# Optimization experiments

Hardware: AMD Instinct MI355X
Metric: run time of the kernel (lower is better)

Reference implementation:

```python
import jax, jax.numpy as jnp
import numpy as np

EMBED_DIM = 1024
NUM_HEADS = 16
HEAD_DIM = EMBED_DIM // NUM_HEADS
# Source divides by scale = head_dim**-0.5, i.e. multiplies logits by sqrt(head_dim).
INV_SCALE = float(HEAD_DIM) ** 0.5


def setup_inputs() -> dict:
    key = jax.random.key(0)
    ks = jax.random.split(key, 9)
    E = EMBED_DIM
    s = 1.0 / np.sqrt(E)
    x = jax.random.normal(ks[0], (2, 2048, E), dtype=jnp.float32)
    Wq = jax.random.uniform(ks[1], (E, E), jnp.float32, -s, s)
    bq = jax.random.uniform(ks[2], (E,), jnp.float32, -s, s)
    Wk = jax.random.uniform(ks[3], (E, E), jnp.float32, -s, s)
    bk = jax.random.uniform(ks[4], (E,), jnp.float32, -s, s)
    Wv = jax.random.uniform(ks[5], (E, E), jnp.float32, -s, s)
    bv = jax.random.uniform(ks[6], (E,), jnp.float32, -s, s)
    Wo = jax.random.uniform(ks[7], (E, E), jnp.float32, -s, s)
    bo = jax.random.uniform(ks[8], (E,), jnp.float32, -s, s)
    return {"x": x, "Wq": Wq, "bq": bq, "Wk": Wk, "bk": bk,
            "Wv": Wv, "bv": bv, "Wo": Wo, "bo": bo}


def reference(x, Wq, bq, Wk, bk, Wv, bv, Wo, bo):
    B, N, C = x.shape
    H, D = NUM_HEADS, HEAD_DIM
    # nn.Linear: y = x @ W.T + b
    q = (x @ Wq.T + bq).reshape(B, N, H, D).transpose(0, 2, 1, 3)  # [B,H,N,D]
    k = (x @ Wk.T + bk).reshape(B, N, H, D).transpose(0, 2, 1, 3)
    v = (x @ Wv.T + bv).reshape(B, N, H, D).transpose(0, 2, 1, 3)
    # Faithful to source: logits = QK^T / (head_dim**-0.5) = QK^T * sqrt(head_dim)
    logits = jnp.einsum('bhnd,bhmd->bhnm', q, k) * INV_SCALE  # [B,H,N,N]
    attn = jax.nn.softmax(logits, axis=-1)
    h = jnp.einsum('bhnm,bhmd->bhnd', attn, v)  # [B,H,N,D]
    concat_h = h.transpose(0, 2, 1, 3).reshape(B, N, C)
    return concat_h @ Wo.T + bo
```

## Files before the change

kernel.cpp:

```cpp
#include <hip/hip_runtime.h>
#include <math.h>

#define B_ 2
#define N_ 2048
#define E_ 1024
#define H_ 16
#define D_ 64

typedef unsigned short US;
typedef _Float16 h16x8 __attribute__((ext_vector_type(8)));
typedef _Float16 h16x4 __attribute__((ext_vector_type(4)));
typedef __fp16 fp16x2 __attribute__((ext_vector_type(2)));
typedef float f32x4 __attribute__((ext_vector_type(4)));
#define MFMA16F(a,b,c)  __builtin_amdgcn_mfma_f32_16x16x32_f16(a,b,c,0,0,0)
#define MFMA161(a,b,c)  __builtin_amdgcn_mfma_f32_16x16x16f16(a,b,c,0,0,0)
#define SCL  11.5415603828f

union HU { _Float16 h; US u; };
__device__ __forceinline__ US f2h(float f){ HU x; x.h = (_Float16)f; return x.u; }
__device__ __forceinline__ unsigned pkrtz(float a, float b){
  union { fp16x2 h; unsigned u; } x;
  x.h = __builtin_amdgcn_cvt_pkrtz(a, b);
  return x.u;
}

union U8 { US u[8]; uint4 v; };
union U4 { US u[4]; uint2 v; };
union UPA { unsigned u[2]; h16x4 h; };

__device__ __forceinline__ void glds16(const US* g, US* l){
  __builtin_amdgcn_global_load_lds(
    (const __attribute__((address_space(1))) unsigned int*)(const void*)g,
    (__attribute__((address_space(3))) unsigned int*)(void*)l, 16, 0, 0);
}

__global__ __launch_bounds__(256) void conv_all(
    const float* __restrict__ x,
    const float* __restrict__ w0, const float* __restrict__ w1,
    const float* __restrict__ w2, const float* __restrict__ w3,
    US* __restrict__ xh, US* __restrict__ Wall)
{
  const int id = blockIdx.x;
  const float* s; US* d; size_t off;
  if (id < 2048) { s = x; d = xh; off = (size_t)id*2048; }
  else {
    int j = id - 2048, wsel = j>>9;
    off = (size_t)(j&511)*2048;
    s = (wsel==0)?w0:(wsel==1)?w1:(wsel==2)?w2:w3;
    d = Wall + (size_t)wsel*1048576;
  }
  size_t i = off + (size_t)threadIdx.x*8;
  float f[8];
  *(float4*)&f[0] = *(const float4*)&s[i];
  *(float4*)&f[4] = *(const float4*)&s[i+4];
  U8 h;
  #pragma unroll
  for (int j=0;j<8;++j) h.u[j] = f2h(f[j]);
  *(uint4*)&d[i] = h.v;
}

__global__ __launch_bounds__(256,3) void qkv_gemm(
    const US* __restrict__ A, const US* __restrict__ Wall,
    const float* __restrict__ bq, const float* __restrict__ bk, const float* __restrict__ bv,
    US* __restrict__ Qf, US* __restrict__ Kf, US* __restrict__ Vtb)
{
  __shared__ __align__(16) US sA[128*32];
  __shared__ __align__(16) US sW[128*32];
  const int z = blockIdx.z;
  const US* W = Wall + (size_t)z*1048576;
  const float* bias = (z==0)?bq:(z==1)?bk:bv;

  const int t = threadIdx.x;
  const int w = t>>6, lane = t&63;
  const int q = lane>>4, c = lane&15;
  const int mq = (w>>1)*64, nq = (w&1)*64;
  const int gm0 = blockIdx.y*128, gn0 = blockIdx.x*128;
  const int r16 = lane>>2, seg = lane&3;

  f32x4 acc[4][4] = {};
  for (int kb = 0; kb < 1024; kb += 32) {
    #pragma unroll
    for (int p=0;p<2;++p){
      int rb = (w*2+p)*16;
      glds16(&A[(size_t)(gm0 + rb + r16)*1024 + kb + seg*8], &sA[rb*32]);
      glds16(&W[(size_t)(gn0 + rb + r16)*1024 + kb + seg*8], &sW[rb*32]);
    }
    __syncthreads();
    h16x8 af[4], wf[4];
    #pragma unroll
    for (int rt=0;rt<4;++rt) af[rt] = *(const h16x8*)&sA[(mq+rt*16+c)*32 + q*8];
    #pragma unroll
    for (int ct=0;ct<4;++ct) wf[ct] = *(const h16x8*)&sW[(nq+ct*16+c)*32 + q*8];
    #pragma unroll
    for (int rt=0;rt<4;++rt)
      #pragma unroll
      for (int ct=0;ct<4;++ct)
        acc[rt][ct] = MFMA16F(af[rt], wf[ct], acc[rt][ct]);
    __syncthreads();
  }
  #pragma unroll
  for (int rt=0;rt<4;++rt)
  #pragma unroll
  for (int ct=0;ct<4;++ct) {
    int col = gn0 + nq + ct*16 + c;
    float bv_ = bias[col];
    int rowb = gm0 + mq + rt*16 + q*4;
    int hh = col>>6, d = col & 63;
    if (z==2) {
      int b = rowb>>11, n = rowb & (N_-1);
      U4 pk;
      #pragma unroll
      for (int r=0;r<4;++r) pk.u[r] = f2h(acc[rt][ct][r] + bv_);
      *(uint2*)&Vtb[((size_t)(b*H_+hh)*D_ + d)*N_ + n] = pk.v;
    } else {
      US* dst = (z==0) ? Qf : Kf;
      #pragma unroll
      for (int r=0;r<4;++r) {
        int row = rowb + r;
        float v = acc[rt][ct][r] + bv_;
        if (z==0) v *= SCL;
        int b = row>>11, n = row & (N_-1);
        dst[((size_t)(b*H_+hh)*N_+n)*D_ + d] = f2h(v);
      }
    }
  }
}

__global__ __launch_bounds__(256,8) void o_gemm(
    const US* __restrict__ A, const US* __restrict__ W,
    const float* __restrict__ bias, float* __restrict__ out)
{
  __shared__ __align__(16) US sA[64*32];
  __shared__ __align__(16) US sW[64*32];
  const int t = threadIdx.x;
  const int w = t>>6, lane = t&63;
  const int q = lane>>4, c = lane&15;
  const int wr = (w>>1)*32, wc = (w&1)*32;
  const int gm0 = blockIdx.y*64, gn0 = blockIdx.x*64;
  const int r4 = lane>>2, seg = lane&3;

  f32x4 acc[2][2] = {};
  for (int kb = 0; kb < 1024; kb += 32) {
    glds16(&A[(size_t)(gm0 + w*16 + r4)*1024 + kb + seg*8], &sA[(w*16)*32]);
    glds16(&W[(size_t)(gn0 + w*16 + r4)*1024 + kb + seg*8], &sW[(w*16)*32]);
    __syncthreads();
    h16x8 af[2], wf[2];
    #pragma unroll
    for (int rt=0;rt<2;++rt) af[rt] = *(const h16x8*)&sA[(wr+rt*16+c)*32 + q*8];
    #pragma unroll
    for (int ct=0;ct<2;++ct) wf[ct] = *(const h16x8*)&sW[(wc+ct*16+c)*32 + q*8];
    #pragma unroll
    for (int rt=0;rt<2;++rt)
      #pragma unroll
      for (int ct=0;ct<2;++ct)
        acc[rt][ct] = MFMA16F(af[rt], wf[ct], acc[rt][ct]);
    __syncthreads();
  }
  #pragma unroll
  for (int rt=0; rt<2; ++rt)
  #pragma unroll
  for (int ct=0; ct<2; ++ct) {
    int col = gn0 + wc + ct*16 + c;
    float bv_ = bias[col];
    int rowb = gm0 + wr + rt*16 + q*4;
    #pragma unroll
    for (int r=0;r<4;++r)
      out[(size_t)(rowb+r)*1024 + col] = acc[rt][ct][r] + bv_;
  }
}

#define KSTR2 72
#define VSTR  136
__global__ __launch_bounds__(512,4) void attn(
    const US* __restrict__ Qf, const US* __restrict__ Kf, const US* __restrict__ Vt,
    US* __restrict__ Hout)
{
  __shared__ __align__(16) US sK [2][128*KSTR2];
  __shared__ __align__(16) US sVt[2][64*VSTR];
  const int t = threadIdx.x;
  const int w = t>>6, lane = t&63, q = lane>>4, c = lane&15;
  const int id = blockIdx.x;
  const int bh = ((id & 7) << 2) | ((id >> 3) & 3);
  const int n0 = (id >> 5) * 128;
  const US* Kp = Kf + (size_t)bh * (N_*D_);
  const US* Vp = Vt + (size_t)bh * (D_*N_);

  const size_t qoff = (size_t)bh*(N_*D_) + (size_t)(n0 + w*16 + c)*D_;
  h16x8 qb0 = *(const h16x8*)&Qf[qoff + q*8];
  h16x8 qb1 = *(const h16x8*)&Qf[qoff + 32 + q*8];
  h16x4 vones;
  #pragma unroll
  for (int j=0;j<4;++j) vones[j] = (_Float16)1.0f;

  float mi = -INFINITY;
  f32x4 o[5] = {};

  const int kr = t>>3, kc8 = (t&7)*8;
  const int vr = t>>4, vc8 = (t&15)*8;

  #pragma unroll
  for (int p=0;p<2;++p){
    int r = p*64 + kr;
    *(uint4*)&sK[0][r*KSTR2 + kc8] = *(const uint4*)&Kp[(size_t)r*D_ + kc8];
  }
  #pragma unroll
  for (int p=0;p<2;++p){
    int r = p*32 + vr;
    *(uint4*)&sVt[0][r*VSTR + vc8] = *(const uint4*)&Vp[(size_t)r*N_ + vc8];
  }
  __syncthreads();

  for (int mt=0; mt<16; ++mt) {
    const int cur = mt&1;
    uint4 kreg[2], vreg[2];
    if (mt < 15){
      const int m1 = (mt+1)*128;
      #pragma unroll
      for (int p=0;p<2;++p)
        kreg[p] = *(const uint4*)&Kp[(size_t)(m1 + p*64 + kr)*D_ + kc8];
      #pragma unroll
      for (int p=0;p<2;++p)
        vreg[p] = *(const uint4*)&Vp[(size_t)(p*32 + vr)*N_ + m1 + vc8];
    }

    f32x4 s[8];
    __builtin_amdgcn_s_setprio(1);
    #pragma unroll
    for (int f=0; f<8; ++f){
      h16x8 k0 = *(const h16x8*)&sK[cur][(f*16+c)*KSTR2 + q*8];
      h16x8 k1 = *(const h16x8*)&sK[cur][(f*16+c)*KSTR2 + 32 + q*8];
      f32x4 sv = {};
      sv = MFMA16F(k0, qb0, sv);
      sv = MFMA16F(k1, qb1, sv);
      s[f] = sv;
    }
    __builtin_amdgcn_s_setprio(0);

    f32x4 t1;
    #pragma unroll
    for (int j=0;j<4;++j){
      float a = fmaxf(fmaxf(s[0][j],s[1][j]),s[2][j]);
      float b = fmaxf(fmaxf(s[3][j],s[4][j]),s[5][j]);
      float d = fmaxf(fmaxf(s[6][j],s[7][j]),a);
      t1[j] = fmaxf(b,d);
    }
    float v = fmaxf(fmaxf(t1[0],t1[1]), fmaxf(t1[2],t1[3]));
    v = fmaxf(v, __shfl_xor(v, 16));
    v = fmaxf(v, __shfl_xor(v, 32));
    if (!__all(v <= mi + 8.0f)) {
      float mnew = fmaxf(mi, v);
      float alpha = exp2f(mi - mnew);
      float ar[4];
      #pragma unroll
      for (int r=0; r<4; ++r) ar[r] = __shfl(alpha, q*4+r);
      #pragma unroll
      for (int dt=0; dt<5; ++dt){
        o[dt][0]*=ar[0]; o[dt][1]*=ar[1]; o[dt][2]*=ar[2]; o[dt][3]*=ar[3];
      }
      mi = mnew;
    }
    #pragma unroll
    for (int f=0; f<8; ++f){
      float p0 = exp2f(s[f][0]-mi);
      float p1 = exp2f(s[f][1]-mi);
      float p2 = exp2f(s[f][2]-mi);
      float p3 = exp2f(s[f][3]-mi);
      UPA pa;
      pa.u[0] = pkrtz(p0, p1);
      pa.u[1] = pkrtz(p2, p3);
      h16x4 pah = pa.h;
      __builtin_amdgcn_s_setprio(1);
      #pragma unroll
      for (int dt=0; dt<4; ++dt){
        h16x4 vf = *(const h16x4*)&sVt[cur][(dt*16+c)*VSTR + f*16 + q*4];
        o[dt] = MFMA161(pah, vf, o[dt]);
      }
      o[4] = MFMA161(pah, vones, o[4]);
      __builtin_amdgcn_s_setprio(0);
    }

    if (mt < 15){
      #pragma unroll
      for (int p=0;p<2;++p)
        *(uint4*)&sK[cur^1][(p*64+kr)*KSTR2 + kc8] = kreg[p];
      #pragma unroll
      for (int p=0;p<2;++p)
        *(uint4*)&sVt[cur^1][(p*32+vr)*VSTR + vc8] = vreg[p];
    }
    __syncthreads();
  }

  const int b = bh>>4, hh = bh&15;
  float ir[4];
  #pragma unroll
  for (int r=0; r<4; ++r) ir[r] = 1.0f / o[4][r];
  #pragma unroll
  for (int dt=0; dt<4; ++dt){
    #pragma unroll
    for (int r=0; r<4; ++r){
      int n = n0 + w*16 + q*4 + r;
      int d = dt*16 + c;
      Hout[((size_t)(b*N_+n)*H_+hh)*D_ + d] = f2h(o[dt][r] * ir[r]);
    }
  }
}

extern "C" void kernel_launch(void* const* d_in, const int* in_sizes, int n_in,
                              void* d_out, int out_size, void* d_ws, size_t ws_size,
                              hipStream_t stream)
{
  const float* x  = (const float*)d_in[0];
  const float* Wq = (const float*)d_in[1];
  const float* bq = (const float*)d_in[2];
  const float* Wk = (const float*)d_in[3];
  const float* bk = (const float*)d_in[4];
  const float* Wv = (const float*)d_in[5];
  const float* bv = (const float*)d_in[6];
  const float* Wo = (const float*)d_in[7];
  const float* bo = (const float*)d_in[8];
  US* ws  = (US*)d_ws;
  const size_t M1 = 1048576;
  US* xh   = ws;
  US* Wall = ws + 4*M1;
  US* Qf   = ws + 8*M1;
  US* Kf   = ws + 12*M1;
  US* Vtb  = ws + 16*M1;
  US* Hf   = ws + 20*M1;

  conv_all<<<4096, 256, 0, stream>>>(x, Wq, Wk, Wv, Wo, xh, Wall);
  qkv_gemm<<<dim3(8,32,3), 256, 0, stream>>>(xh, Wall, bq, bk, bv, Qf, Kf, Vtb);
  attn<<<512, 512, 0, stream>>>(Qf, Kf, Vtb, Hf);
  o_gemm<<<dim3(16,64), 256, 0, stream>>>(Hf, Wall + 3*M1, bo, (float*)d_out);
}
```

Baseline: 206.2 us.

## Software-pipeline QK^T of the next tile with PV of the current tile

The attention loop now computes the score MFMAs for the first K tile before the loop. Inside the loop it computes exponentials into a packed array, stores the prefetched K/V into the other LDS buffer, then issues the next tile's QK^T MFMAs back-to-back with the current tile's PV MFMAs. The aim is to decouple the softmax VALU work from the dependent MFMA chain and keep the matrix units busier under one high-priority region. In exchange it adds a second __syncthreads per iteration and more live registers (eight packed P fragments plus the next S tile), which may lower occupancy.

```diff
diff --git a/kernel.cpp b/kernel.cpp
--- a/kernel.cpp
+++ b/kernel.cpp
@@ -198,21 +198,34 @@
   const int kr = t>>3, kc8 = (t&7)*8;
   const int vr = t>>4, vc8 = (t&15)*8;
 
-  #pragma unroll
-  for (int p=0;p<2;++p){
-    int r = p*64 + kr;
-    *(uint4*)&sK[0][r*KSTR2 + kc8] = *(const uint4*)&Kp[(size_t)r*D_ + kc8];
-  }
-  #pragma unroll
-  for (int p=0;p<2;++p){
-    int r = p*32 + vr;
-    *(uint4*)&sVt[0][r*VSTR + vc8] = *(const uint4*)&Vp[(size_t)r*N_ + vc8];
-  }
+  uint4 kreg[2], vreg[2];
+  #pragma unroll
+  for (int p=0;p<2;++p)
+    kreg[p] = *(const uint4*)&Kp[(size_t)(p*64 + kr)*D_ + kc8];
+  #pragma unroll
+  for (int p=0;p<2;++p)
+    vreg[p] = *(const uint4*)&Vp[(size_t)(p*32 + vr)*N_ + vc8];
+  #pragma unroll
+  for (int p=0;p<2;++p)
+    *(uint4*)&sK[0][(p*64+kr)*KSTR2 + kc8] = kreg[p];
+  #pragma unroll
+  for (int p=0;p<2;++p)
+    *(uint4*)&sVt[0][(p*32+vr)*VSTR + vc8] = vreg[p];
   __syncthreads();
+
+  f32x4 s[8];
+  #pragma unroll
+  for (int f=0; f<8; ++f){
+    h16x8 k0 = *(const h16x8*)&sK[0][(f*16+c)*KSTR2 + q*8];
+    h16x8 k1 = *(const h16x8*)&sK[0][(f*16+c)*KSTR2 + 32 + q*8];
+    f32x4 sv = {};
+    sv = MFMA16F(k0, qb0, sv);
+    sv = MFMA16F(k1, qb1, sv);
+    s[f] = sv;
+  }
 
   for (int mt=0; mt<16; ++mt) {
     const int cur = mt&1;
-    uint4 kreg[2], vreg[2];
     if (mt < 15){
       const int m1 = (mt+1)*128;
       #pragma unroll
@@ -222,19 +235,6 @@
       for (int p=0;p<2;++p)
         vreg[p] = *(const uint4*)&Vp[(size_t)(p*32 + vr)*N_ + m1 + vc8];
     }
-
-    f32x4 s[8];
-    __builtin_amdgcn_s_setprio(1);
-    #pragma unroll
-    for (int f=0; f<8; ++f){
-      h16x8 k0 = *(const h16x8*)&sK[cur][(f*16+c)*KSTR2 + q*8];
-      h16x8 k1 = *(const h16x8*)&sK[cur][(f*16+c)*KSTR2 + 32 + q*8];
-      f32x4 sv = {};
-      sv = MFMA16F(k0, qb0, sv);
-      sv = MFMA16F(k1, qb1, sv);
-      s[f] = sv;
-    }
-    __builtin_amdgcn_s_setprio(0);
 
     f32x4 t1;
     #pragma unroll
@@ -259,35 +259,52 @@
       }
       mi = mnew;
     }
+    UPA pa_[8];
     #pragma unroll
     for (int f=0; f<8; ++f){
       float p0 = exp2f(s[f][0]-mi);
       float p1 = exp2f(s[f][1]-mi);
       float p2 = exp2f(s[f][2]-mi);
       float p3 = exp2f(s[f][3]-mi);
-      UPA pa;
-      pa.u[0] = pkrtz(p0, p1);
-      pa.u[1] = pkrtz(p2, p3);
-      h16x4 pah = pa.h;
-      __builtin_amdgcn_s_setprio(1);
+      pa_[f].u[0] = pkrtz(p0, p1);
+      pa_[f].u[1] = pkrtz(p2, p3);
+    }
+
+    __syncthreads();
+
+    if (mt < 15){
+      #pragma unroll
+      for (int p=0;p<2;++p)
+        *(uint4*)&sK[cur^1][(p*64+kr)*KSTR2 + kc8] = kreg[p];
+      #pragma unroll
+      for (int p=0;p<2;++p)
+        *(uint4*)&sVt[cur^1][(p*32+vr)*VSTR + vc8] = vreg[p];
+    }
+    __syncthreads();
+
+    __builtin_amdgcn_s_setprio(1);
+    if (mt < 15){
+      #pragma unroll
+      for (int f=0; f<8; ++f){
+        h16x8 k0 = *(const h16x8*)&sK[cur^1][(f*16+c)*KSTR2 + q*8];
+        h16x8 k1 = *(const h16x8*)&sK[cur^1][(f*16+c)*KSTR2 + 32 + q*8];
+        f32x4 sv = {};
+        sv = MFMA16F(k0, qb0, sv);
+        sv = MFMA16F(k1, qb1, sv);
+        s[f] = sv;
+      }
+    }
+    #pragma unroll
+    for (int f=0; f<8; ++f){
+      h16x4 pah = pa_[f].h;
       #pragma unroll
       for (int dt=0; dt<4; ++dt){
         h16x4 vf = *(const h16x4*)&sVt[cur][(dt*16+c)*VSTR + f*16 + q*4];
         o[dt] = MFMA161(pah, vf, o[dt]);
       }
       o[4] = MFMA161(pah, vones, o[4]);
-      __builtin_amdgcn_s_setprio(0);
-    }
-
-    if (mt < 15){
-      #pragma unroll
-      for (int p=0;p<2;++p)
-        *(uint4*)&sK[cur^1][(p*64+kr)*KSTR2 + kc8] = kreg[p];
-      #pragma unroll
-      for (int p=0;p<2;++p)
-        *(uint4*)&sVt[cur^1][(p*32+vr)*VSTR + vc8] = vreg[p];
-    }
-    __syncthreads();
+    }
+    __builtin_amdgcn_s_setprio(0);
   }
 
   const int b = bh>>4, hh = bh&15;
```

Result: slower. 239.5 us (+16.1%).

## Widen QKV GEMM K-tile with XOR swizzle; read K directly from global in attention

Applied to the files above, without the earlier changes.

The QKV projection GEMM now stages 64-wide K slices instead of 32, which halves the number of barrier pairs per output tile. It uses an XOR swizzle on the 16-byte segment index to avoid LDS bank conflicts in the unpadded layout. The attention kernel drops the shared-memory double buffer for K and loads K fragments straight from global memory (L2/cache) into MFMA operands. This cuts LDS footprint and store traffic, but risks exposing global-load latency in the QK^T phase, since each wave now reads K independently.

```diff
diff --git a/kernel.cpp b/kernel.cpp
--- a/kernel.cpp
+++ b/kernel.cpp
@@ -64,8 +64,8 @@
     const float* __restrict__ bq, const float* __restrict__ bk, const float* __restrict__ bv,
     US* __restrict__ Qf, US* __restrict__ Kf, US* __restrict__ Vtb)
 {
-  __shared__ __align__(16) US sA[128*32];
-  __shared__ __align__(16) US sW[128*32];
+  __shared__ __align__(16) US sA[128*64];
+  __shared__ __align__(16) US sW[128*64];
   const int z = blockIdx.z;
   const US* W = Wall + (size_t)z*1048576;
   const float* bias = (z==0)?bq:(z==1)?bk:bv;
@@ -75,27 +75,33 @@
   const int q = lane>>4, c = lane&15;
   const int mq = (w>>1)*64, nq = (w&1)*64;
   const int gm0 = blockIdx.y*128, gn0 = blockIdx.x*128;
-  const int r16 = lane>>2, seg = lane&3;
+  const int r8 = lane>>3, seg = lane&7;
+  const int sseg = (seg ^ r8) << 3;
 
   f32x4 acc[4][4] = {};
-  for (int kb = 0; kb < 1024; kb += 32) {
-    #pragma unroll
-    for (int p=0;p<2;++p){
-      int rb = (w*2+p)*16;
-      glds16(&A[(size_t)(gm0 + rb + r16)*1024 + kb + seg*8], &sA[rb*32]);
-      glds16(&W[(size_t)(gn0 + rb + r16)*1024 + kb + seg*8], &sW[rb*32]);
-    }
-    __syncthreads();
-    h16x8 af[4], wf[4];
-    #pragma unroll
-    for (int rt=0;rt<4;++rt) af[rt] = *(const h16x8*)&sA[(mq+rt*16+c)*32 + q*8];
-    #pragma unroll
-    for (int ct=0;ct<4;++ct) wf[ct] = *(const h16x8*)&sW[(nq+ct*16+c)*32 + q*8];
-    #pragma unroll
-    for (int rt=0;rt<4;++rt)
+  for (int kb = 0; kb < 1024; kb += 64) {
+    #pragma unroll
+    for (int p=0;p<4;++p){
+      int rb = (w*4+p)*8;
+      glds16(&A[(size_t)(gm0 + rb + r8)*1024 + kb + sseg], &sA[rb*64]);
+      glds16(&W[(size_t)(gn0 + rb + r8)*1024 + kb + sseg], &sW[rb*64]);
+    }
+    __syncthreads();
+    #pragma unroll
+    for (int kc=0;kc<2;++kc){
+      h16x8 af[4], wf[4];
+      #pragma unroll
+      for (int rt=0;rt<4;++rt)
+        af[rt] = *(const h16x8*)&sA[(mq+rt*16+c)*64 + (((kc*4+q) ^ (c&7))<<3)];
       #pragma unroll
       for (int ct=0;ct<4;++ct)
-        acc[rt][ct] = MFMA16F(af[rt], wf[ct], acc[rt][ct]);
+        wf[ct] = *(const h16x8*)&sW[(nq+ct*16+c)*64 + (((kc*4+q) ^ (c&7))<<3)];
+      #pragma unroll
+      for (int rt=0;rt<4;++rt)
+        #pragma unroll
+        for (int ct=0;ct<4;++ct)
+          acc[rt][ct] = MFMA16F(af[rt], wf[ct], acc[rt][ct]);
+    }
     __syncthreads();
   }
   #pragma unroll
@@ -169,13 +175,11 @@
   }
 }
 
-#define KSTR2 72
 #define VSTR  136
 __global__ __launch_bounds__(512,4) void attn(
     const US* __restrict__ Qf, const US* __restrict__ Kf, const US* __restrict__ Vt,
     US* __restrict__ Hout)
 {
-  __shared__ __align__(16) US sK [2][128*KSTR2];
   __shared__ __align__(16) US sVt[2][64*VSTR];
   const int t = threadIdx.x;
   const int w = t>>6, lane = t&63, q = lane>>4, c = lane&15;
@@ -195,14 +199,8 @@
   float mi = -INFINITY;
   f32x4 o[5] = {};
 
-  const int kr = t>>3, kc8 = (t&7)*8;
   const int vr = t>>4, vc8 = (t&15)*8;
 
-  #pragma unroll
-  for (int p=0;p<2;++p){
-    int r = p*64 + kr;
-    *(uint4*)&sK[0][r*KSTR2 + kc8] = *(const uint4*)&Kp[(size_t)r*D_ + kc8];
-  }
   #pragma unroll
   for (int p=0;p<2;++p){
     int r = p*32 + vr;
@@ -212,23 +210,21 @@
 
   for (int mt=0; mt<16; ++mt) {
     const int cur = mt&1;
-    uint4 kreg[2], vreg[2];
+    uint4 vreg[2];
     if (mt < 15){
       const int m1 = (mt+1)*128;
       #pragma unroll
       for (int p=0;p<2;++p)
-        kreg[p] = *(const uint4*)&Kp[(size_t)(m1 + p*64 + kr)*D_ + kc8];
-      #pragma unroll
-      for (int p=0;p<2;++p)
         vreg[p] = *(const uint4*)&Vp[(size_t)(p*32 + vr)*N_ + m1 + vc8];
     }
 
+    const US* Krow = Kp + (size_t)(mt*128)*D_;
     f32x4 s[8];
     __builtin_amdgcn_s_setprio(1);
     #pragma unroll
     for (int f=0; f<8; ++f){
-      h16x8 k0 = *(const h16x8*)&sK[cur][(f*16+c)*KSTR2 + q*8];
-      h16x8 k1 = *(const h16x8*)&sK[cur][(f*16+c)*KSTR2 + 32 + q*8];
+      h16x8 k0 = *(const h16x8*)&Krow[(f*16+c)*D_ + q*8];
+      h16x8 k1 = *(const h16x8*)&Krow[(f*16+c)*D_ + 32 + q*8];
       f32x4 sv = {};
       sv = MFMA16F(k0, qb0, sv);
       sv = MFMA16F(k1, qb1, sv);
@@ -280,9 +276,6 @@
     }
 
     if (mt < 15){
-      #pragma unroll
-      for (int p=0;p<2;++p)
-        *(uint4*)&sK[cur^1][(p*64+kr)*KSTR2 + kc8] = kreg[p];
       #pragma unroll
       for (int p=0;p<2;++p)
         *(uint4*)&sVt[cur^1][(p*32+vr)*VSTR + vc8] = vreg[p];
```

Result: slower. 297.1 us (+44.1%).

## Fold running max into MFMA accumulator and permute V smem for wide reads

Applied to the files above, without the earlier changes.

Seeds the QK^T MFMA accumulator with -mi so scores come out already shifted, removing a per-element subtraction before exp2 on the common no-rescale path. The online-softmax logic is reorganised so mi tracks accumulated shifts, with a separate branch for rescaling. V^T is stored into shared memory in a permuted order so each PV step does one 16-byte LDS read that feeds two MFMAs instead of two 8-byte reads. This adds code duplication and split stores to shared memory, and changes how the rescale threshold is applied relative to the running max.

```diff
diff --git a/kernel.cpp b/kernel.cpp
--- a/kernel.cpp
+++ b/kernel.cpp
@@ -192,11 +192,13 @@
   #pragma unroll
   for (int j=0;j<4;++j) vones[j] = (_Float16)1.0f;
 
-  float mi = -INFINITY;
+  float mi = 0.0f;
   f32x4 o[5] = {};
 
   const int kr = t>>3, kc8 = (t&7)*8;
-  const int vr = t>>4, vc8 = (t&15)*8;
+  const int vr = t>>4, kidx = t&15;
+  const int vf_ = kidx>>1, vqa = (kidx&1)<<1;
+  const int vp0 = vqa*32 + vf_*4, vp1 = (vqa+1)*32 + vf_*4;
 
   #pragma unroll
   for (int p=0;p<2;++p){
@@ -206,7 +208,9 @@
   #pragma unroll
   for (int p=0;p<2;++p){
     int r = p*32 + vr;
-    *(uint4*)&sVt[0][r*VSTR + vc8] = *(const uint4*)&Vp[(size_t)r*N_ + vc8];
+    uint4 vv = *(const uint4*)&Vp[(size_t)r*N_ + kidx*8];
+    *(uint2*)&sVt[0][r*VSTR + vp0] = make_uint2(vv.x, vv.y);
+    *(uint2*)&sVt[0][r*VSTR + vp1] = make_uint2(vv.z, vv.w);
   }
   __syncthreads();
 
@@ -220,17 +224,17 @@
         kreg[p] = *(const uint4*)&Kp[(size_t)(m1 + p*64 + kr)*D_ + kc8];
       #pragma unroll
       for (int p=0;p<2;++p)
-        vreg[p] = *(const uint4*)&Vp[(size_t)(p*32 + vr)*N_ + m1 + vc8];
+        vreg[p] = *(const uint4*)&Vp[(size_t)(p*32 + vr)*N_ + m1 + kidx*8];
     }
 
     f32x4 s[8];
+    const f32x4 mC = {-mi, -mi, -mi, -mi};
     __builtin_amdgcn_s_setprio(1);
     #pragma unroll
     for (int f=0; f<8; ++f){
       h16x8 k0 = *(const h16x8*)&sK[cur][(f*16+c)*KSTR2 + q*8];
       h16x8 k1 = *(const h16x8*)&sK[cur][(f*16+c)*KSTR2 + 32 + q*8];
-      f32x4 sv = {};
-      sv = MFMA16F(k0, qb0, sv);
+      f32x4 sv = MFMA16F(k0, qb0, mC);
       sv = MFMA16F(k1, qb1, sv);
       s[f] = sv;
     }
@@ -247,9 +251,9 @@
     float v = fmaxf(fmaxf(t1[0],t1[1]), fmaxf(t1[2],t1[3]));
     v = fmaxf(v, __shfl_xor(v, 16));
     v = fmaxf(v, __shfl_xor(v, 32));
-    if (!__all(v <= mi + 8.0f)) {
-      float mnew = fmaxf(mi, v);
-      float alpha = exp2f(mi - mnew);
+    if (mt == 0 || !__all(v <= 8.0f)) {
+      float dm = (mt == 0) ? v : fmaxf(0.0f, v);
+      float alpha = (mt == 0) ? 0.0f : exp2f(-dm);
       float ar[4];
       #pragma unroll
       for (int r=0; r<4; ++r) ar[r] = __shfl(alpha, q*4+r);
@@ -257,26 +261,48 @@
       for (int dt=0; dt<5; ++dt){
         o[dt][0]*=ar[0]; o[dt][1]*=ar[1]; o[dt][2]*=ar[2]; o[dt][3]*=ar[3];
       }
-      mi = mnew;
-    }
-    #pragma unroll
-    for (int f=0; f<8; ++f){
-      float p0 = exp2f(s[f][0]-mi);
-      float p1 = exp2f(s[f][1]-mi);
-      float p2 = exp2f(s[f][2]-mi);
-      float p3 = exp2f(s[f][3]-mi);
-      UPA pa;
-      pa.u[0] = pkrtz(p0, p1);
-      pa.u[1] = pkrtz(p2, p3);
-      h16x4 pah = pa.h;
-      __builtin_amdgcn_s_setprio(1);
-      #pragma unroll
-      for (int dt=0; dt<4; ++dt){
-        h16x4 vf = *(const h16x4*)&sVt[cur][(dt*16+c)*VSTR + f*16 + q*4];
-        o[dt] = MFMA161(pah, vf, o[dt]);
-      }
-      o[4] = MFMA161(pah, vones, o[4]);
-      __builtin_amdgcn_s_setprio(0);
+      mi += dm;
+      #pragma unroll
+      for (int fp=0; fp<4; ++fp){
+        UPA pa0, pa1;
+        pa0.u[0] = pkrtz(exp2f(s[2*fp][0]-dm),   exp2f(s[2*fp][1]-dm));
+        pa0.u[1] = pkrtz(exp2f(s[2*fp][2]-dm),   exp2f(s[2*fp][3]-dm));
+        pa1.u[0] = pkrtz(exp2f(s[2*fp+1][0]-dm), exp2f(s[2*fp+1][1]-dm));
+        pa1.u[1] = pkrtz(exp2f(s[2*fp+1][2]-dm), exp2f(s[2*fp+1][3]-dm));
+        __builtin_amdgcn_s_setprio(1);
+        #pragma unroll
+        for (int dt=0; dt<4; ++dt){
+          h16x8 v8 = *(const h16x8*)&sVt[cur][(dt*16+c)*VSTR + q*32 + fp*8];
+          h16x4 v0 = __builtin_shufflevector(v8, v8, 0,1,2,3);
+          h16x4 v1 = __builtin_shufflevector(v8, v8, 4,5,6,7);
+          o[dt] = MFMA161(pa0.h, v0, o[dt]);
+          o[dt] = MFMA161(pa1.h, v1, o[dt]);
+        }
+        o[4] = MFMA161(pa0.h, vones, o[4]);
+        o[4] = MFMA161(pa1.h, vones, o[4]);
+        __builtin_amdgcn_s_setprio(0);
+      }
+    } else {
+      #pragma unroll
+      for (int fp=0; fp<4; ++fp){
+        UPA pa0, pa1;
+        pa0.u[0] = pkrtz(exp2f(s[2*fp][0]),   exp2f(s[2*fp][1]));
+        pa0.u[1] = pkrtz(exp2f(s[2*fp][2]),   exp2f(s[2*fp][3]));
+        pa1.u[0] = pkrtz(exp2f(s[2*fp+1][0]), exp2f(s[2*fp+1][1]));
+        pa1.u[1] = pkrtz(exp2f(s[2*fp+1][2]), exp2f(s[2*fp+1][3]));
+        __builtin_amdgcn_s_setprio(1);
+        #pragma unroll
+        for (int dt=0; dt<4; ++dt){
+          h16x8 v8 = *(const h16x8*)&sVt[cur][(dt*16+c)*VSTR + q*32 + fp*8];
+          h16x4 v0 = __builtin_shufflevector(v8, v8, 0,1,2,3);
+          h16x4 v1 = __builtin_shufflevector(v8, v8, 4,5,6,7);
+          o[dt] = MFMA161(pa0.h, v0, o[dt]);
+          o[dt] = MFMA161(pa1.h, v1, o[dt]);
+        }
+        o[4] = MFMA161(pa0.h, vones, o[4]);
+        o[4] = MFMA161(pa1.h, vones, o[4]);
+        __builtin_amdgcn_s_setprio(0);
+      }
     }
 
     if (mt < 15){
@@ -284,8 +310,10 @@
       for (int p=0;p<2;++p)
         *(uint4*)&sK[cur^1][(p*64+kr)*KSTR2 + kc8] = kreg[p];
       #pragma unroll
-      for (int p=0;p<2;++p)
-        *(uint4*)&sVt[cur^1][(p*32+vr)*VSTR + vc8] = vreg[p];
+      for (int p=0;p<2;++p){
+        *(uint2*)&sVt[cur^1][(p*32+vr)*VSTR + vp0] = make_uint2(vreg[p].x, vreg[p].y);
+        *(uint2*)&sVt[cur^1][(p*32+vr)*VSTR + vp1] = make_uint2(vreg[p].z, vreg[p].w);
+      }
     }
     __syncthreads();
   }
```

After: 216.9 us. 5.2% more time.
